# Kernel tuning notes

Hardware: AMD Instinct MI355X
Metric: run time of the kernel (lower is better)

## Reference

```python
import jax, jax.numpy as jnp
import numpy as np

D_MODEL = 1024
B, T = 4, 2048
NEG = -1000000000.0


def setup_inputs() -> dict:
    key = jax.random.key(0)
    kq, kk, kv = jax.random.split(key, 3)
    query = jax.random.normal(kq, (B, T, D_MODEL), dtype=jnp.float32)
    k = jax.random.normal(kk, (B, T, D_MODEL), dtype=jnp.float32)
    value = jax.random.normal(kv, (B, T, D_MODEL), dtype=jnp.float32)
    # causal mask: 1.0 where attention is disallowed (strictly upper triangular)
    mask = jnp.triu(jnp.ones((T, T), dtype=jnp.float32), k=1)
    return {"query": query, "key": k, "value": value, "mask": mask}


def reference(query, key, value, mask):
    # dk = sqrt(1/d_model); logits = QK^T / dk  (i.e. * sqrt(d_model)) -- faithful to source
    dk = jnp.sqrt(jnp.float32(1.0) / jnp.float32(D_MODEL))
    attn_logits = jnp.einsum("btc,bsc->bts", query, key) / dk
    attn_logits = attn_logits + mask * NEG  # mask broadcasts over batch
    score = jax.nn.softmax(attn_logits, axis=-1)
    attention = jnp.einsum("bts,bsc->btc", score, value)
    return attention
```

## Files before the change

kernel.cpp:

```cpp
#include <hip/hip_runtime.h>

#define BB 4
#define TT 2048
#define DD 1024
#define SCALE 32.0f
#define NTILE 136
#define L2E 1.4426950408889634f

typedef _Float16 f16;
typedef __attribute__((ext_vector_type(4))) _Float16 half4v;
typedef __attribute__((ext_vector_type(8))) _Float16 half8v;
typedef __attribute__((ext_vector_type(16))) float f32x16;

typedef const __attribute__((address_space(1))) unsigned int* gas_u32;
typedef __attribute__((address_space(3))) unsigned int* las_u32;

static __device__ inline void gload16(const void* g, void* l) {
    __builtin_amdgcn_global_load_lds((gas_u32)g, (las_u32)l, 16, 0, 0);
}

static __device__ inline half8v ld_frag(const f16* p) {
    half4v a = *(const half4v*)p;
    half4v b = *(const half4v*)(p + 4);
    half8v r;
    r[0] = a[0]; r[1] = a[1]; r[2] = a[2]; r[3] = a[3];
    r[4] = b[0]; r[5] = b[1]; r[6] = b[2]; r[7] = b[3];
    return r;
}


__global__ __launch_bounds__(256) void repack_qk(const float* __restrict__ Q,
                                                 const float* __restrict__ K,
                                                 f16* __restrict__ Qt,
                                                 f16* __restrict__ Kt) {
    __shared__ char rl[32768];
    int bid = blockIdx.x;
    int which = bid >> 10, b = (bid >> 8) & 3, mi = (bid >> 4) & 15, ks4 = bid & 15;
    const float* src = which ? K : Q;
    f16* dst = which ? Kt : Qt;
    float sc = which ? 1.0f : SCALE;

    int tid = threadIdx.x;
    int r = tid >> 1, h = tid & 1;
    const float* p = src + ((size_t)(b * TT + mi * 128 + r)) * DD + ks4 * 64 + h * 32;
#pragma unroll
    for (int j = 0; j < 4; ++j) {
        float4 x0 = *(const float4*)(p + j * 8);
        float4 x1 = *(const float4*)(p + j * 8 + 4);
        float vv[8] = {x0.x, x0.y, x0.z, x0.w, x1.x, x1.y, x1.z, x1.w};
        half8v hi, lo;
#pragma unroll
        for (int e = 0; e < 8; ++e) {
            float x = vv[e] * sc;
            f16 hh = (f16)x;
            hi[e] = hh;
            lo[e] = (f16)(x - (float)hh);
        }
        int ckl = h * 2 + (j >> 1);
        int shalf = j & 1;
        *(half8v*)(rl + ckl * 8192 + shalf * 2048 + r * 16) = hi;
        *(half8v*)(rl + ckl * 8192 + (2 + shalf) * 2048 + r * 16) = lo;
    }
    __syncthreads();
    char* gout = (char*)dst + ((size_t)((b * 16 + mi) * 64 + ks4 * 4)) * 8192 + tid * 128;
#pragma unroll
    for (int q = 0; q < 8; ++q)
        *(float4*)(gout + q * 16) = *(float4*)(rl + tid * 128 + q * 16);
}

__global__ __launch_bounds__(256) void transpose_v(const float* __restrict__ V,
                                                   f16* __restrict__ Vt) {
    __shared__ float Vs[64][129];
    int bid = blockIdx.x;
    int b = bid >> 8, kb = (bid >> 3) & 31, nj = bid & 7;
    const float* src = V + ((size_t)(b * TT + kb * 64)) * DD + nj * 128;
    int tid = threadIdx.x;
#pragma unroll
    for (int it = 0; it < 8; ++it) {
        int f4 = it * 256 + tid;
        int row = f4 >> 5, c4 = f4 & 31;
        float4 x = *(const float4*)(src + (size_t)row * DD + c4 * 4);
        Vs[row][c4 * 4 + 0] = x.x;
        Vs[row][c4 * 4 + 1] = x.y;
        Vs[row][c4 * 4 + 2] = x.z;
        Vs[row][c4 * 4 + 3] = x.w;
    }
    __syncthreads();
#pragma unroll
    for (int qq = 0; qq < 4; ++qq) {
        int q = tid * 4 + qq;
        int ckl = q >> 9, s = (q >> 7) & 3, n = q & 127;
        half8v hv;
#pragma unroll
        for (int e = 0; e < 8; ++e) hv[e] = (f16)Vs[ckl * 32 + s * 8 + e][n];
        char* out = (char*)Vt + ((size_t)((b * 8 + nj) * 64 + kb * 2 + ckl)) * 8192
                    + s * 2048 + n * 16;
        *(half8v*)out = hv;
    }
}

__global__ __launch_bounds__(256, 3) void k1_qk3(const f16* __restrict__ Qt,
                                                 const f16* __restrict__ Kt,
                                                 float* __restrict__ S) {
    __shared__ char lds[32768];

    int bid0 = blockIdx.x;
    int bid = (bid0 & 7) * (BB * NTILE / 8) + (bid0 >> 3);
    int b = bid / NTILE, rr0 = bid % NTILE;
    int mi = 0;
    while ((mi + 1) * (mi + 2) / 2 <= rr0) ++mi;
    int nj = rr0 - mi * (mi + 1) / 2;

    const char* Abase = (const char*)Qt + ((size_t)((b * 16 + mi) * 64)) * 8192;
    const char* Bbase = (const char*)Kt + ((size_t)((b * 16 + nj) * 64)) * 8192;
    float* Sb = S + (size_t)b * TT * TT + (size_t)(mi * 128) * TT + nj * 128;

    int tid = threadIdx.x;
    int lane = tid & 63;
    int wv = tid >> 6;
    int l31 = lane & 31, lhi = lane >> 5;
    int wrow = wv >> 1, wcol = wv & 1;

    int aoff[2], boff[2];
#pragma unroll
    for (int f = 0; f < 2; ++f) {
        int ra = wrow * 64 + f * 32 + l31;
        int rb = wcol * 64 + f * 32 + l31;
        aoff[f] = lhi * 2048 + ra * 16;
        boff[f] = lhi * 2048 + rb * 16;
    }
    int lane_go = wv * 2048 + lane * 16;
    int lane_lo = wv * 2048;

    f32x16 acc[2][2] = {};

#define K1_STAGE(CK, BUF)                                                       \
    {                                                                           \
        const char* ga = Abase + (size_t)(CK) * 8192 + lane_go;                 \
        const char* gb = Bbase + (size_t)(CK) * 8192 + lane_go;                 \
        char* la = lds + (BUF) * 16384 + lane_lo;                               \
        char* lb = la + 8192;                                                   \
        gload16(ga, la);                                                        \
        gload16(ga + 1024, la + 1024);                                          \
        gload16(gb, lb);                                                        \
        gload16(gb + 1024, lb + 1024);                                          \
    }

    K1_STAGE(0, 0);
    int cur = 0;
    for (int ck = 0; ck < 64; ++ck) {
        __syncthreads();
        if (ck + 1 < 64) K1_STAGE(ck + 1, cur ^ 1);
        const char* As = lds + cur * 16384;
        const char* Bs = As + 8192;
        half8v ah[2], al[2], bh[2], bl[2];
#pragma unroll
        for (int f = 0; f < 2; ++f) {
            ah[f] = *(const half8v*)(As + aoff[f]);
            al[f] = *(const half8v*)(As + aoff[f] + 4096);
            bh[f] = *(const half8v*)(Bs + boff[f]);
            bl[f] = *(const half8v*)(Bs + boff[f] + 4096);
        }
#pragma unroll
        for (int fm = 0; fm < 2; ++fm)
#pragma unroll
            for (int fn = 0; fn < 2; ++fn) {
                acc[fm][fn] = __builtin_amdgcn_mfma_f32_32x32x16_f16(ah[fm], bh[fn], acc[fm][fn], 0, 0, 0);
                acc[fm][fn] = __builtin_amdgcn_mfma_f32_32x32x16_f16(ah[fm], bl[fn], acc[fm][fn], 0, 0, 0);
                acc[fm][fn] = __builtin_amdgcn_mfma_f32_32x32x16_f16(al[fm], bh[fn], acc[fm][fn], 0, 0, 0);
            }
        cur ^= 1;
    }
#undef K1_STAGE
#pragma unroll
    for (int fm = 0; fm < 2; ++fm)
#pragma unroll
        for (int fn = 0; fn < 2; ++fn)
#pragma unroll
            for (int g = 0; g < 16; ++g) {
                int rr = (g & 3) + 8 * (g >> 2) + 4 * lhi;
                int row = wrow * 64 + fm * 32 + rr;
                int col = wcol * 64 + fn * 32 + l31;
                Sb[(size_t)row * TT + col] = acc[fm][fn][g];
            }
}

__global__ __launch_bounds__(256) void k1b3(const float* __restrict__ S,
                                            f16* __restrict__ Pt) {
    __shared__ float red[4];
    int rowid = blockIdx.x;
    int b = rowid >> 11, t = rowid & (TT - 1);
    const float* Sr = S + ((size_t)b * TT + t) * TT;
    int tid = threadIdx.x;
    int nv = t + 1;
    int mi = t >> 7, r = t & 127;
    int rowend = (mi + 1) << 7;
    int c = tid * 8;
    bool act = c < rowend;

    float v[8] = {0, 0, 0, 0, 0, 0, 0, 0};
    if (act) {
        float4 x0 = *(const float4*)(Sr + c);
        float4 x1 = *(const float4*)(Sr + c + 4);
        v[0] = x0.x; v[1] = x0.y; v[2] = x0.z; v[3] = x0.w;
        v[4] = x1.x; v[5] = x1.y; v[6] = x1.z; v[7] = x1.w;
    }

    float m = -3.0e38f;
    if (act) {
#pragma unroll
        for (int j = 0; j < 8; ++j)
            if (c + j < nv) m = fmaxf(m, v[j]);
    }
#pragma unroll
    for (int o = 32; o > 0; o >>= 1) m = fmaxf(m, __shfl_xor(m, o));
    if ((tid & 63) == 0) red[tid >> 6] = m;
    __syncthreads();
    m = fmaxf(fmaxf(red[0], red[1]), fmaxf(red[2], red[3]));
    __syncthreads();

    float e[8];
    float s = 0.f;
#pragma unroll
    for (int j = 0; j < 8; ++j) {
        e[j] = (act && c + j < nv) ? exp2f((v[j] - m) * L2E) : 0.0f;
        s += e[j];
    }
#pragma unroll
    for (int o = 32; o > 0; o >>= 1) s += __shfl_xor(s, o);
    if ((tid & 63) == 0) red[tid >> 6] = s;
    __syncthreads();
    s = red[0] + red[1] + red[2] + red[3];
    float inv = 1.0f / s;

    if (act) {
        half8v hv;
#pragma unroll
        for (int j = 0; j < 8; ++j) hv[j] = (f16)(e[j] * inv);
        int ck = c >> 5, sl = (c >> 3) & 3;
        char* dst = (char*)Pt + ((size_t)((b * 16 + mi) * 64 + ck)) * 8192
                    + sl * 2048 + r * 16;
        *(half8v*)dst = hv;
    }
}

__global__ __launch_bounds__(256, 2) void k2_pv3(const f16* __restrict__ Pt,
                                                 const f16* __restrict__ Vt,
                                                 float* __restrict__ O) {
    __shared__ char lds[49152];

    int bid0 = blockIdx.x;
    int bid = (bid0 & 7) * 32 + (bid0 >> 3);
    int b = bid >> 6, mi = (bid >> 2) & 15, nj2 = bid & 3;
    int kc = (mi + 1) * 4;

    const char* Abase = (const char*)Pt + ((size_t)((b * 16 + mi) * 64)) * 8192;
    const char* B0base = (const char*)Vt + ((size_t)((b * 8 + nj2 * 2) * 64)) * 8192;
    const char* B1base = (const char*)Vt + ((size_t)((b * 8 + nj2 * 2 + 1) * 64)) * 8192;
    float* Ob = O + (size_t)b * TT * DD + (size_t)(mi * 128) * DD + nj2 * 256;

    int tid = threadIdx.x;
    int lane = tid & 63;
    int wv = tid >> 6;
    int l31 = lane & 31, lhi = lane >> 5;
    int wr = wv >> 1, wc = wv & 1;

    f32x16 acc[2][4] = {};
    int lane16 = lane * 16;

#define K2_STAGE(CK, BUF)                                                       \
    {                                                                           \
        size_t gck = (size_t)(CK) * 8192;                                       \
        char* lb = lds + (BUF) * 24576;                                         \
        _Pragma("unroll") for (int i = 0; i < 6; ++i) {                         \
            int off = (i * 4 + wv) * 1024;                                      \
            const char* gsrc = (off < 8192) ? (Abase + gck + off)               \
                             : (off < 16384) ? (B0base + gck + off - 8192)      \
                                             : (B1base + gck + off - 16384);    \
            gload16(gsrc + lane16, lb + off);                                   \
        }                                                                       \
    }

    K2_STAGE(0, 0);
    int cur = 0;
    for (int ck = 0; ck < kc; ++ck) {
        __syncthreads();
        if (ck + 1 < kc) K2_STAGE(ck + 1, cur ^ 1);
        const char* As = lds + cur * 24576;
        const char* Bs = As + 8192 + wc * 8192;
#pragma unroll
        for (int ks = 0; ks < 2; ++ks) {
            int slot = (ks * 2 + lhi) * 2048;
            half8v a0 = *(const half8v*)(As + slot + (wr * 64 + l31) * 16);
            half8v a1 = *(const half8v*)(As + slot + (wr * 64 + 32 + l31) * 16);
            half8v b0 = *(const half8v*)(Bs + slot + (l31) * 16);
            half8v b1 = *(const half8v*)(Bs + slot + (32 + l31) * 16);
            half8v b2 = *(const half8v*)(Bs + slot + (64 + l31) * 16);
            half8v b3 = *(const half8v*)(Bs + slot + (96 + l31) * 16);
            acc[0][0] = __builtin_amdgcn_mfma_f32_32x32x16_f16(a0, b0, acc[0][0], 0, 0, 0);
            acc[0][1] = __builtin_amdgcn_mfma_f32_32x32x16_f16(a0, b1, acc[0][1], 0, 0, 0);
            acc[0][2] = __builtin_amdgcn_mfma_f32_32x32x16_f16(a0, b2, acc[0][2], 0, 0, 0);
            acc[0][3] = __builtin_amdgcn_mfma_f32_32x32x16_f16(a0, b3, acc[0][3], 0, 0, 0);
            acc[1][0] = __builtin_amdgcn_mfma_f32_32x32x16_f16(a1, b0, acc[1][0], 0, 0, 0);
            acc[1][1] = __builtin_amdgcn_mfma_f32_32x32x16_f16(a1, b1, acc[1][1], 0, 0, 0);
            acc[1][2] = __builtin_amdgcn_mfma_f32_32x32x16_f16(a1, b2, acc[1][2], 0, 0, 0);
            acc[1][3] = __builtin_amdgcn_mfma_f32_32x32x16_f16(a1, b3, acc[1][3], 0, 0, 0);
        }
        cur ^= 1;
    }
#undef K2_STAGE
#pragma unroll
    for (int fm = 0; fm < 2; ++fm)
#pragma unroll
        for (int fn = 0; fn < 4; ++fn)
#pragma unroll
            for (int g = 0; g < 16; ++g) {
                int rr = (g & 3) + 8 * (g >> 2) + 4 * lhi;
                int row = wr * 64 + fm * 32 + rr;
                int col = wc * 128 + fn * 32 + l31;
                Ob[(size_t)row * DD + col] = acc[fm][fn][g];
            }
}

__global__ __launch_bounds__(256, 2) void k1_qk(const float* __restrict__ Q,
                                                const float* __restrict__ Kmat,
                                                float* __restrict__ S) {
    __shared__ f16 Ah[128][36], Al[128][36], Bh[128][36], Bl[128][36];
    int bid = blockIdx.x;
    int b = bid / NTILE, r = bid % NTILE;
    int mi = 0;
    while ((mi + 1) * (mi + 2) / 2 <= r) ++mi;
    int nj = r - mi * (mi + 1) / 2;
    const float* Qb = Q + ((size_t)b * TT + (size_t)mi * 128) * DD;
    const float* Kb = Kmat + ((size_t)b * TT + (size_t)nj * 128) * DD;
    float* Sb = S + (size_t)b * TT * TT + (size_t)(mi * 128) * TT + nj * 128;
    int tid = threadIdx.x;
    int lane = tid & 63;
    int wave = tid >> 6;
    int l31 = lane & 31, lhi = lane >> 5;
    int wrow = wave >> 1, wcol = wave & 1;
    int r0 = tid >> 1;
    int c0 = (tid & 1) * 16;
    f32x16 acc[2][2] = {};
    float4 abuf[4], bbuf[4];
#pragma unroll
    for (int j = 0; j < 4; ++j) {
        abuf[j] = *(const float4*)(Qb + (size_t)r0 * DD + c0 + 4 * j);
        bbuf[j] = *(const float4*)(Kb + (size_t)r0 * DD + c0 + 4 * j);
    }
    for (int ch = 0; ch < DD / 32; ++ch) {
        __syncthreads();
#pragma unroll
        for (int j = 0; j < 4; ++j) {
            float4 a = abuf[j], bq = bbuf[j];
            float ax[4] = {a.x * SCALE, a.y * SCALE, a.z * SCALE, a.w * SCALE};
            float bx[4] = {bq.x, bq.y, bq.z, bq.w};
            half4v ahv, alv, bhv, blv;
#pragma unroll
            for (int e = 0; e < 4; ++e) {
                f16 h = (f16)ax[e];
                ahv[e] = h;
                alv[e] = (f16)(ax[e] - (float)h);
                f16 g = (f16)bx[e];
                bhv[e] = g;
                blv[e] = (f16)(bx[e] - (float)g);
            }
            *(half4v*)&Ah[r0][c0 + 4 * j] = ahv;
            *(half4v*)&Al[r0][c0 + 4 * j] = alv;
            *(half4v*)&Bh[r0][c0 + 4 * j] = bhv;
            *(half4v*)&Bl[r0][c0 + 4 * j] = blv;
        }
        __syncthreads();
        if (ch + 1 < DD / 32) {
            int ck = (ch + 1) * 32;
#pragma unroll
            for (int j = 0; j < 4; ++j) {
                abuf[j] = *(const float4*)(Qb + (size_t)r0 * DD + ck + c0 + 4 * j);
                bbuf[j] = *(const float4*)(Kb + (size_t)r0 * DD + ck + c0 + 4 * j);
            }
        }
#pragma unroll
        for (int ks = 0; ks < 2; ++ks) {
            int kb = ks * 16 + lhi * 8;
            half8v ahf[2], alf[2], bhf[2], blf[2];
#pragma unroll
            for (int f = 0; f < 2; ++f) {
                ahf[f] = ld_frag(&Ah[wrow * 64 + f * 32 + l31][kb]);
                alf[f] = ld_frag(&Al[wrow * 64 + f * 32 + l31][kb]);
                bhf[f] = ld_frag(&Bh[wcol * 64 + f * 32 + l31][kb]);
                blf[f] = ld_frag(&Bl[wcol * 64 + f * 32 + l31][kb]);
            }
#pragma unroll
            for (int fm = 0; fm < 2; ++fm)
#pragma unroll
                for (int fn = 0; fn < 2; ++fn) {
                    acc[fm][fn] = __builtin_amdgcn_mfma_f32_32x32x16_f16(ahf[fm], bhf[fn], acc[fm][fn], 0, 0, 0);
                    acc[fm][fn] = __builtin_amdgcn_mfma_f32_32x32x16_f16(ahf[fm], blf[fn], acc[fm][fn], 0, 0, 0);
                    acc[fm][fn] = __builtin_amdgcn_mfma_f32_32x32x16_f16(alf[fm], bhf[fn], acc[fm][fn], 0, 0, 0);
                }
        }
    }
#pragma unroll
    for (int fm = 0; fm < 2; ++fm)
#pragma unroll
        for (int fn = 0; fn < 2; ++fn)
#pragma unroll
            for (int g = 0; g < 16; ++g) {
                int rr = (g & 3) + 8 * (g >> 2) + 4 * lhi;
                int row = wrow * 64 + fm * 32 + rr;
                int col = wcol * 64 + fn * 32 + l31;
                Sb[(size_t)row * TT + col] = acc[fm][fn][g];
            }
}

__global__ __launch_bounds__(256) void k1b_softmax(const float* __restrict__ S,
                                                   f16* __restrict__ P) {
    __shared__ float red[4];
    int rowid = blockIdx.x;
    int b = rowid >> 11, t = rowid & (TT - 1);
    const float* Sr = S + (size_t)b * TT * TT + (size_t)t * TT;
    f16* Pr = P + (size_t)b * TT * TT + (size_t)t * TT;
    int tid = threadIdx.x;
    int nv = t + 1;
    int rowend = ((t >> 7) + 1) << 7;
    float m = -3.0e38f;
    for (int c = tid; c < nv; c += 256) m = fmaxf(m, Sr[c]);
#pragma unroll
    for (int o = 32; o > 0; o >>= 1) m = fmaxf(m, __shfl_xor(m, o));
    if ((tid & 63) == 0) red[tid >> 6] = m;
    __syncthreads();
    m = fmaxf(fmaxf(red[0], red[1]), fmaxf(red[2], red[3]));
    __syncthreads();
    float s = 0.f;
    for (int c = tid; c < nv; c += 256) s += exp2f((Sr[c] - m) * L2E);
#pragma unroll
    for (int o = 32; o > 0; o >>= 1) s += __shfl_xor(s, o);
    if ((tid & 63) == 0) red[tid >> 6] = s;
    __syncthreads();
    s = red[0] + red[1] + red[2] + red[3];
    float inv = 1.0f / s;
    for (int c = tid; c < rowend; c += 256) {
        float p = (c < nv) ? exp2f((Sr[c] - m) * L2E) * inv : 0.0f;
        Pr[c] = (f16)p;
    }
}

__global__ __launch_bounds__(256, 2) void k2_pv(const f16* __restrict__ P,
                                                const float* __restrict__ V,
                                                float* __restrict__ O) {
    __shared__ f16 Pa[128][36];
    __shared__ f16 Vtt[128][36];
    int bid = blockIdx.x;
    int b = bid >> 7;
    int rest = bid & 127;
    int mi = rest >> 3, nj = rest & 7;
    int kend = (mi + 1) * 128;
    const f16* Pb = P + (size_t)b * TT * TT + (size_t)(mi * 128) * TT;
    const float* Vb = V + (size_t)b * TT * DD + nj * 128;
    float* Ob = O + (size_t)b * TT * DD + (size_t)(mi * 128) * DD + nj * 128;
    int tid = threadIdx.x;
    int lane = tid & 63;
    int wave = tid >> 6;
    int l31 = lane & 31, lhi = lane >> 5;
    int wrow = wave >> 1, wcol = wave & 1;
    f32x16 acc[2][2] = {};
    int pr = tid >> 1, pc = (tid & 1) * 16;
    int vk = tid >> 3, vn = (tid & 7) * 16;
    uint2 pbuf[4];
    float4 vbuf[4];
#pragma unroll
    for (int j = 0; j < 4; ++j) {
        pbuf[j] = *(const uint2*)(Pb + (size_t)pr * TT + pc + 4 * j);
        vbuf[j] = *(const float4*)(Vb + (size_t)vk * DD + vn + 4 * j);
    }
    for (int ck = 0; ck < kend; ck += 32) {
        __syncthreads();
#pragma unroll
        for (int j = 0; j < 4; ++j) {
            *(uint2*)&Pa[pr][pc + 4 * j] = pbuf[j];
            float4 v = vbuf[j];
            float vv[4] = {v.x, v.y, v.z, v.w};
            int n0 = vn + 4 * j;
#pragma unroll
            for (int e = 0; e < 4; ++e) {
                int n = n0 + e;
                Vtt[n][vk ^ ((((unsigned)n >> 4) & 3) << 3)] = (f16)vv[e];
            }
        }
        __syncthreads();
        if (ck + 32 < kend) {
            int cn = ck + 32;
#pragma unroll
            for (int j = 0; j < 4; ++j) {
                pbuf[j] = *(const uint2*)(Pb + (size_t)pr * TT + cn + pc + 4 * j);
                vbuf[j] = *(const float4*)(Vb + (size_t)(cn + vk) * DD + vn + 4 * j);
            }
        }
#pragma unroll
        for (int ks = 0; ks < 2; ++ks) {
            int kb = ks * 16 + lhi * 8;
            half8v paf[2], vbf[2];
#pragma unroll
            for (int f = 0; f < 2; ++f) {
                paf[f] = ld_frag(&Pa[wrow * 64 + f * 32 + l31][kb]);
                int n = wcol * 64 + f * 32 + l31;
                int kbs = kb ^ ((((unsigned)n >> 4) & 3) << 3);
                vbf[f] = ld_frag(&Vtt[n][kbs]);
            }
#pragma unroll
            for (int fm = 0; fm < 2; ++fm)
#pragma unroll
                for (int fn = 0; fn < 2; ++fn)
                    acc[fm][fn] = __builtin_amdgcn_mfma_f32_32x32x16_f16(paf[fm], vbf[fn], acc[fm][fn], 0, 0, 0);
        }
    }
#pragma unroll
    for (int fm = 0; fm < 2; ++fm)
#pragma unroll
        for (int fn = 0; fn < 2; ++fn)
#pragma unroll
            for (int g = 0; g < 16; ++g) {
                int rr = (g & 3) + 8 * (g >> 2) + 4 * lhi;
                int row = wrow * 64 + fm * 32 + rr;
                int col = wcol * 64 + fn * 32 + l31;
                Ob[(size_t)row * DD + col] = acc[fm][fn][g];
            }
}

__global__ __launch_bounds__(256) void fa_fallback(const float* __restrict__ Q,
                                                   const float* __restrict__ Kmat,
                                                   const float* __restrict__ V,
                                                   float* __restrict__ O) {
    __shared__ float qs[DD];
    __shared__ float osum[DD];
    __shared__ float red[4];
    int rowid = blockIdx.x;
    int b = rowid >> 11, t = rowid & (TT - 1);
    const float* q = Q + ((size_t)b * TT + t) * DD;
    int tid = threadIdx.x;
    for (int j = tid; j < DD; j += 256) { qs[j] = q[j] * SCALE; osum[j] = 0.f; }
    __syncthreads();
    float m = -3.0e38f, l = 0.f;
    for (int s = 0; s <= t; ++s) {
        const float* kr = Kmat + ((size_t)b * TT + s) * DD;
        float part = 0.f;
#pragma unroll
        for (int j = 0; j < 4; ++j) part += qs[tid * 4 + j] * kr[tid * 4 + j];
#pragma unroll
        for (int o = 32; o > 0; o >>= 1) part += __shfl_xor(part, o);
        if ((tid & 63) == 0) red[tid >> 6] = part;
        __syncthreads();
        float dot = red[0] + red[1] + red[2] + red[3];
        float mn = fmaxf(m, dot);
        float f = exp2f((m - mn) * 1.44269504f);
        float e = exp2f((dot - mn) * 1.44269504f);
        l = l * f + e;
        const float* vr = V + ((size_t)b * TT + s) * DD;
#pragma unroll
        for (int j = 0; j < 4; ++j) {
            int c = tid * 4 + j;
            osum[c] = osum[c] * f + e * vr[c];
        }
        m = mn;
        __syncthreads();
    }
    float inv = 1.f / l;
    for (int j = tid; j < DD; j += 256) O[((size_t)b * TT + t) * DD + j] = osum[j] * inv;
}

extern "C" void kernel_launch(void* const* d_in, const int* in_sizes, int n_in,
                              void* d_out, int out_size, void* d_ws, size_t ws_size,
                              hipStream_t stream) {
    const float* Q = (const float*)d_in[0];
    const float* K = (const float*)d_in[1];
    const float* V = (const float*)d_in[2];
    float* O = (float*)d_out;

    const size_t MB = 1024 * 1024;
    const size_t QT_B = 32 * MB, KT_B = 32 * MB, VT_B = 16 * MB, S_B = 64 * MB;
    const size_t FULL = QT_B + KT_B + VT_B + S_B;

    size_t sbytes = (size_t)BB * TT * TT * 4;
    size_t pbytes = (size_t)BB * TT * TT * 2;

    if (ws_size >= FULL) {
        f16* Qt = (f16*)d_ws;
        f16* Kt = (f16*)((char*)d_ws + QT_B);
        f16* Vt = (f16*)((char*)d_ws + QT_B + KT_B);
        float* S = (float*)((char*)d_ws + QT_B + KT_B + VT_B);
        f16* Pt = (f16*)d_ws;
        hipLaunchKernelGGL(repack_qk, dim3(2048), dim3(256), 0, stream, Q, K, Qt, Kt);
        hipLaunchKernelGGL(transpose_v, dim3(1024), dim3(256), 0, stream, V, Vt);
        hipLaunchKernelGGL(k1_qk3, dim3(BB * NTILE), dim3(256), 0, stream, Qt, Kt, S);
        hipLaunchKernelGGL(k1b3, dim3(BB * TT), dim3(256), 0, stream, S, Pt);
        hipLaunchKernelGGL(k2_pv3, dim3(256), dim3(256), 0, stream, Pt, Vt, O);
    } else if (ws_size >= sbytes + pbytes) {
        float* S = (float*)d_ws;
        f16* P = (f16*)((char*)d_ws + sbytes);
        hipLaunchKernelGGL(k1_qk, dim3(BB * NTILE), dim3(256), 0, stream, Q, K, S);
        hipLaunchKernelGGL(k1b_softmax, dim3(BB * TT), dim3(256), 0, stream, S, P);
        hipLaunchKernelGGL(k2_pv, dim3(BB * 16 * 8), dim3(256), 0, stream, P, V, O);
    } else {
        hipLaunchKernelGGL(fa_fallback, dim3(BB * TT), dim3(256), 0, stream, Q, K, V, O);
    }
}
```

Before: 171.6 us.

## Split K reduction across two wave groups in QK and PV GEMMs

Both GEMM kernels now launch 512 threads per block, and the two halves of the waves each handle half of the reduction dimension. Their partial accumulators are combined through LDS before the store. PV also moves to 128x128 output tiles with twice as many blocks, which gives more waves per CU for the few, uneven causal tiles. The cost is extra LDS traffic and a barrier for the final reduction, plus 64KB of LDS per block, which may limit how many blocks fit on a CU.

Result: no change. 170.8 us (-0.5%).

```diff
diff --git a/kernel.cpp b/kernel.cpp
--- a/kernel.cpp
+++ b/kernel.cpp
@@ -99,10 +99,10 @@
     }
 }
 
-__global__ __launch_bounds__(256, 3) void k1_qk3(const f16* __restrict__ Qt,
+__global__ __launch_bounds__(512, 4) void k1_qk4(const f16* __restrict__ Qt,
                                                  const f16* __restrict__ Kt,
                                                  float* __restrict__ S) {
-    __shared__ char lds[32768];
+    __shared__ char lds[65536];
 
     int bid0 = blockIdx.x;
     int bid = (bid0 & 7) * (BB * NTILE / 8) + (bid0 >> 3);
@@ -118,27 +118,30 @@
     int tid = threadIdx.x;
     int lane = tid & 63;
     int wv = tid >> 6;
+    int kh = wv >> 2;
+    int wq = wv & 3;
     int l31 = lane & 31, lhi = lane >> 5;
-    int wrow = wv >> 1, wcol = wv & 1;
+    int wrow = wq >> 1, wcol = wq & 1;
 
     int aoff[2], boff[2];
 #pragma unroll
     for (int f = 0; f < 2; ++f) {
-        int ra = wrow * 64 + f * 32 + l31;
-        int rb = wcol * 64 + f * 32 + l31;
-        aoff[f] = lhi * 2048 + ra * 16;
-        boff[f] = lhi * 2048 + rb * 16;
-    }
-    int lane_go = wv * 2048 + lane * 16;
-    int lane_lo = wv * 2048;
+        aoff[f] = lhi * 2048 + (wrow * 64 + f * 32 + l31) * 16;
+        boff[f] = lhi * 2048 + (wcol * 64 + f * 32 + l31) * 16;
+    }
+    int lane_go = wq * 2048 + lane * 16;
+    int lane_lo = wq * 2048;
+    char* lds_h = lds + kh * 32768;
+    const char* Ab = Abase + (size_t)kh * 32 * 8192;
+    const char* Bb = Bbase + (size_t)kh * 32 * 8192;
 
     f32x16 acc[2][2] = {};
 
-#define K1_STAGE(CK, BUF)                                                       \
+#define K1_STAGE(IT, BUF)                                                       \
     {                                                                           \
-        const char* ga = Abase + (size_t)(CK) * 8192 + lane_go;                 \
-        const char* gb = Bbase + (size_t)(CK) * 8192 + lane_go;                 \
-        char* la = lds + (BUF) * 16384 + lane_lo;                               \
+        const char* ga = Ab + (size_t)(IT) * 8192 + lane_go;                    \
+        const char* gb = Bb + (size_t)(IT) * 8192 + lane_go;                    \
+        char* la = lds_h + (BUF) * 16384 + lane_lo;                             \
         char* lb = la + 8192;                                                   \
         gload16(ga, la);                                                        \
         gload16(ga + 1024, la + 1024);                                          \
@@ -148,10 +151,10 @@
 
     K1_STAGE(0, 0);
     int cur = 0;
-    for (int ck = 0; ck < 64; ++ck) {
-        __syncthreads();
-        if (ck + 1 < 64) K1_STAGE(ck + 1, cur ^ 1);
-        const char* As = lds + cur * 16384;
+    for (int it = 0; it < 32; ++it) {
+        __syncthreads();
+        if (it + 1 < 32) K1_STAGE(it + 1, cur ^ 1);
+        const char* As = lds_h + cur * 16384;
         const char* Bs = As + 8192;
         half8v ah[2], al[2], bh[2], bl[2];
 #pragma unroll
@@ -172,17 +175,34 @@
         cur ^= 1;
     }
 #undef K1_STAGE
-#pragma unroll
-    for (int fm = 0; fm < 2; ++fm)
-#pragma unroll
-        for (int fn = 0; fn < 2; ++fn)
-#pragma unroll
-            for (int g = 0; g < 16; ++g) {
-                int rr = (g & 3) + 8 * (g >> 2) + 4 * lhi;
-                int row = wrow * 64 + fm * 32 + rr;
-                int col = wcol * 64 + fn * 32 + l31;
-                Sb[(size_t)row * TT + col] = acc[fm][fn][g];
-            }
+
+    __syncthreads();
+    if (kh) {
+#pragma unroll
+        for (int fm = 0; fm < 2; ++fm)
+#pragma unroll
+            for (int fn = 0; fn < 2; ++fn)
+#pragma unroll
+                for (int g = 0; g < 16; ++g)
+                    *(float*)(lds + wq * 16384 + (fm * 2 + fn) * 4096 + g * 256 + lane * 4)
+                        = acc[fm][fn][g];
+    }
+    __syncthreads();
+    if (!kh) {
+#pragma unroll
+        for (int fm = 0; fm < 2; ++fm)
+#pragma unroll
+            for (int fn = 0; fn < 2; ++fn)
+#pragma unroll
+                for (int g = 0; g < 16; ++g) {
+                    float v = acc[fm][fn][g]
+                        + *(const float*)(lds + wq * 16384 + (fm * 2 + fn) * 4096 + g * 256 + lane * 4);
+                    int rr = (g & 3) + 8 * (g >> 2) + 4 * lhi;
+                    int row = wrow * 64 + fm * 32 + rr;
+                    int col = wcol * 64 + fn * 32 + l31;
+                    Sb[(size_t)row * TT + col] = v;
+                }
+    }
 }
 
 __global__ __launch_bounds__(256) void k1b3(const float* __restrict__ S,
@@ -244,82 +264,104 @@
     }
 }
 
-__global__ __launch_bounds__(256, 2) void k2_pv3(const f16* __restrict__ Pt,
+__global__ __launch_bounds__(512, 4) void k2_pv4(const f16* __restrict__ Pt,
                                                  const f16* __restrict__ Vt,
                                                  float* __restrict__ O) {
-    __shared__ char lds[49152];
+    __shared__ char lds[65536];
 
     int bid0 = blockIdx.x;
-    int bid = (bid0 & 7) * 32 + (bid0 >> 3);
-    int b = bid >> 6, mi = (bid >> 2) & 15, nj2 = bid & 3;
-    int kc = (mi + 1) * 4;
+    int bid = (bid0 & 7) * 64 + (bid0 >> 3);
+    int b = bid >> 7, mi = (bid >> 3) & 15, nj = bid & 7;
+    int kch = (mi + 1) * 2;
 
     const char* Abase = (const char*)Pt + ((size_t)((b * 16 + mi) * 64)) * 8192;
-    const char* B0base = (const char*)Vt + ((size_t)((b * 8 + nj2 * 2) * 64)) * 8192;
-    const char* B1base = (const char*)Vt + ((size_t)((b * 8 + nj2 * 2 + 1) * 64)) * 8192;
-    float* Ob = O + (size_t)b * TT * DD + (size_t)(mi * 128) * DD + nj2 * 256;
+    const char* Bbase = (const char*)Vt + ((size_t)((b * 8 + nj) * 64)) * 8192;
+    float* Ob = O + (size_t)b * TT * DD + (size_t)(mi * 128) * DD + nj * 128;
 
     int tid = threadIdx.x;
     int lane = tid & 63;
     int wv = tid >> 6;
+    int kh = wv >> 2;
+    int wq = wv & 3;
     int l31 = lane & 31, lhi = lane >> 5;
-    int wr = wv >> 1, wc = wv & 1;
-
-    f32x16 acc[2][4] = {};
-    int lane16 = lane * 16;
-
-#define K2_STAGE(CK, BUF)                                                       \
+    int wrow = wq >> 1, wcol = wq & 1;
+
+    int arow[2], brow[2];
+#pragma unroll
+    for (int f = 0; f < 2; ++f) {
+        arow[f] = (wrow * 64 + f * 32 + l31) * 16;
+        brow[f] = (wcol * 64 + f * 32 + l31) * 16;
+    }
+    int lane_go = wq * 2048 + lane * 16;
+    int lane_lo = wq * 2048;
+    char* lds_h = lds + kh * 32768;
+    const char* Ab = Abase + (size_t)kh * kch * 8192;
+    const char* Bb = Bbase + (size_t)kh * kch * 8192;
+
+    f32x16 acc[2][2] = {};
+
+#define K2_STAGE(IT, BUF)                                                       \
     {                                                                           \
-        size_t gck = (size_t)(CK) * 8192;                                       \
-        char* lb = lds + (BUF) * 24576;                                         \
-        _Pragma("unroll") for (int i = 0; i < 6; ++i) {                         \
-            int off = (i * 4 + wv) * 1024;                                      \
-            const char* gsrc = (off < 8192) ? (Abase + gck + off)               \
-                             : (off < 16384) ? (B0base + gck + off - 8192)      \
-                                             : (B1base + gck + off - 16384);    \
-            gload16(gsrc + lane16, lb + off);                                   \
-        }                                                                       \
+        const char* ga = Ab + (size_t)(IT) * 8192 + lane_go;                    \
+        const char* gb = Bb + (size_t)(IT) * 8192 + lane_go;                    \
+        char* la = lds_h + (BUF) * 16384 + lane_lo;                             \
+        char* lb = la + 8192;                                                   \
+        gload16(ga, la);                                                        \
+        gload16(ga + 1024, la + 1024);                                          \
+        gload16(gb, lb);                                                        \
+        gload16(gb + 1024, lb + 1024);                                          \
     }
 
     K2_STAGE(0, 0);
     int cur = 0;
-    for (int ck = 0; ck < kc; ++ck) {
-        __syncthreads();
-        if (ck + 1 < kc) K2_STAGE(ck + 1, cur ^ 1);
-        const char* As = lds + cur * 24576;
-        const char* Bs = As + 8192 + wc * 8192;
+    for (int it = 0; it < kch; ++it) {
+        __syncthreads();
+        if (it + 1 < kch) K2_STAGE(it + 1, cur ^ 1);
+        const char* As = lds_h + cur * 16384;
+        const char* Bs = As + 8192;
 #pragma unroll
         for (int ks = 0; ks < 2; ++ks) {
             int slot = (ks * 2 + lhi) * 2048;
-            half8v a0 = *(const half8v*)(As + slot + (wr * 64 + l31) * 16);
-            half8v a1 = *(const half8v*)(As + slot + (wr * 64 + 32 + l31) * 16);
-            half8v b0 = *(const half8v*)(Bs + slot + (l31) * 16);
-            half8v b1 = *(const half8v*)(Bs + slot + (32 + l31) * 16);
-            half8v b2 = *(const half8v*)(Bs + slot + (64 + l31) * 16);
-            half8v b3 = *(const half8v*)(Bs + slot + (96 + l31) * 16);
+            half8v a0 = *(const half8v*)(As + slot + arow[0]);
+            half8v a1 = *(const half8v*)(As + slot + arow[1]);
+            half8v b0 = *(const half8v*)(Bs + slot + brow[0]);
+            half8v b1 = *(const half8v*)(Bs + slot + brow[1]);
             acc[0][0] = __builtin_amdgcn_mfma_f32_32x32x16_f16(a0, b0, acc[0][0], 0, 0, 0);
             acc[0][1] = __builtin_amdgcn_mfma_f32_32x32x16_f16(a0, b1, acc[0][1], 0, 0, 0);
-            acc[0][2] = __builtin_amdgcn_mfma_f32_32x32x16_f16(a0, b2, acc[0][2], 0, 0, 0);
-            acc[0][3] = __builtin_amdgcn_mfma_f32_32x32x16_f16(a0, b3, acc[0][3], 0, 0, 0);
             acc[1][0] = __builtin_amdgcn_mfma_f32_32x32x16_f16(a1, b0, acc[1][0], 0, 0, 0);
             acc[1][1] = __builtin_amdgcn_mfma_f32_32x32x16_f16(a1, b1, acc[1][1], 0, 0, 0);
-            acc[1][2] = __builtin_amdgcn_mfma_f32_32x32x16_f16(a1, b2, acc[1][2], 0, 0, 0);
-            acc[1][3] = __builtin_amdgcn_mfma_f32_32x32x16_f16(a1, b3, acc[1][3], 0, 0, 0);
         }
         cur ^= 1;
     }
 #undef K2_STAGE
-#pragma unroll
-    for (int fm = 0; fm < 2; ++fm)
-#pragma unroll
-        for (int fn = 0; fn < 4; ++fn)
-#pragma unroll
-            for (int g = 0; g < 16; ++g) {
-                int rr = (g & 3) + 8 * (g >> 2) + 4 * lhi;
-                int row = wr * 64 + fm * 32 + rr;
-                int col = wc * 128 + fn * 32 + l31;
-                Ob[(size_t)row * DD + col] = acc[fm][fn][g];
-            }
+
+    __syncthreads();
+    if (kh) {
+#pragma unroll
+        for (int fm = 0; fm < 2; ++fm)
+#pragma unroll
+            for (int fn = 0; fn < 2; ++fn)
+#pragma unroll
+                for (int g = 0; g < 16; ++g)
+                    *(float*)(lds + wq * 16384 + (fm * 2 + fn) * 4096 + g * 256 + lane * 4)
+                        = acc[fm][fn][g];
+    }
+    __syncthreads();
+    if (!kh) {
+#pragma unroll
+        for (int fm = 0; fm < 2; ++fm)
+#pragma unroll
+            for (int fn = 0; fn < 2; ++fn)
+#pragma unroll
+                for (int g = 0; g < 16; ++g) {
+                    float v = acc[fm][fn][g]
+                        + *(const float*)(lds + wq * 16384 + (fm * 2 + fn) * 4096 + g * 256 + lane * 4);
+                    int rr = (g & 3) + 8 * (g >> 2) + 4 * lhi;
+                    int row = wrow * 64 + fm * 32 + rr;
+                    int col = wcol * 64 + fn * 32 + l31;
+                    Ob[(size_t)row * DD + col] = v;
+                }
+    }
 }
 
 __global__ __launch_bounds__(256, 2) void k1_qk(const float* __restrict__ Q,
@@ -591,9 +633,9 @@
         f16* Pt = (f16*)d_ws;
         hipLaunchKernelGGL(repack_qk, dim3(2048), dim3(256), 0, stream, Q, K, Qt, Kt);
         hipLaunchKernelGGL(transpose_v, dim3(1024), dim3(256), 0, stream, V, Vt);
-        hipLaunchKernelGGL(k1_qk3, dim3(BB * NTILE), dim3(256), 0, stream, Qt, Kt, S);
+        hipLaunchKernelGGL(k1_qk4, dim3(BB * NTILE), dim3(512), 0, stream, Qt, Kt, S);
         hipLaunchKernelGGL(k1b3, dim3(BB * TT), dim3(256), 0, stream, S, Pt);
-        hipLaunchKernelGGL(k2_pv3, dim3(256), dim3(256), 0, stream, Pt, Vt, O);
+        hipLaunchKernelGGL(k2_pv4, dim3(512), dim3(512), 0, stream, Pt, Vt, O);
     } else if (ws_size >= sbytes + pbytes) {
         float* S = (float*)d_ws;
         f16* P = (f16*)((char*)d_ws + sbytes);
```

## Triple-buffer QK and PV GEMM loads and halve PV tile width

Applied to the files above, without the earlier changes.

Both GEMM kernels move from a double-buffered LDS pipeline with __syncthreads to a three-stage ring. Loads are issued two chunks ahead, and the code waits with explicit vmcnt counts plus a raw s_barrier, so more global-to-LDS latency can be hidden. The PV kernel's output tile shrinks from 128x256 to 128x128, doubling the grid to 512 blocks, with occupancy raised to 3 blocks per CU. The smaller tile improves load balance on the causal triangle but re-reads P twice as often. The QK kernel's LDS grows to 48KB, which may limit its 3-block occupancy.

Result: faster. 164.1 us (-4.4%).

```diff
diff --git a/kernel.cpp b/kernel.cpp
--- a/kernel.cpp
+++ b/kernel.cpp
@@ -99,10 +99,10 @@
     }
 }
 
-__global__ __launch_bounds__(256, 3) void k1_qk3(const f16* __restrict__ Qt,
+__global__ __launch_bounds__(256, 3) void k1_qk5(const f16* __restrict__ Qt,
                                                  const f16* __restrict__ Kt,
                                                  float* __restrict__ S) {
-    __shared__ char lds[32768];
+    __shared__ char lds[49152];
 
     int bid0 = blockIdx.x;
     int bid = (bid0 & 7) * (BB * NTILE / 8) + (bid0 >> 3);
@@ -124,10 +124,8 @@
     int aoff[2], boff[2];
 #pragma unroll
     for (int f = 0; f < 2; ++f) {
-        int ra = wrow * 64 + f * 32 + l31;
-        int rb = wcol * 64 + f * 32 + l31;
-        aoff[f] = lhi * 2048 + ra * 16;
-        boff[f] = lhi * 2048 + rb * 16;
+        aoff[f] = lhi * 2048 + (wrow * 64 + f * 32 + l31) * 16;
+        boff[f] = lhi * 2048 + (wcol * 64 + f * 32 + l31) * 16;
     }
     int lane_go = wv * 2048 + lane * 16;
     int lane_lo = wv * 2048;
@@ -147,11 +145,15 @@
     }
 
     K1_STAGE(0, 0);
-    int cur = 0;
+    K1_STAGE(1, 1);
+    int cb = 0;
+    int sb = 2;
     for (int ck = 0; ck < 64; ++ck) {
-        __syncthreads();
-        if (ck + 1 < 64) K1_STAGE(ck + 1, cur ^ 1);
-        const char* As = lds + cur * 16384;
+        if (ck < 63) asm volatile("s_waitcnt vmcnt(4)" ::: "memory");
+        else         asm volatile("s_waitcnt vmcnt(0)" ::: "memory");
+        __builtin_amdgcn_s_barrier();
+        if (ck + 2 < 64) K1_STAGE(ck + 2, sb);
+        const char* As = lds + cb * 16384;
         const char* Bs = As + 8192;
         half8v ah[2], al[2], bh[2], bl[2];
 #pragma unroll
@@ -169,7 +171,8 @@
                 acc[fm][fn] = __builtin_amdgcn_mfma_f32_32x32x16_f16(ah[fm], bl[fn], acc[fm][fn], 0, 0, 0);
                 acc[fm][fn] = __builtin_amdgcn_mfma_f32_32x32x16_f16(al[fm], bh[fn], acc[fm][fn], 0, 0, 0);
             }
-        cur ^= 1;
+        cb = (cb == 2) ? 0 : cb + 1;
+        sb = (sb == 2) ? 0 : sb + 1;
     }
 #undef K1_STAGE
 #pragma unroll
@@ -244,80 +247,84 @@
     }
 }
 
-__global__ __launch_bounds__(256, 2) void k2_pv3(const f16* __restrict__ Pt,
+__global__ __launch_bounds__(256, 3) void k2_pv5(const f16* __restrict__ Pt,
                                                  const f16* __restrict__ Vt,
                                                  float* __restrict__ O) {
     __shared__ char lds[49152];
 
     int bid0 = blockIdx.x;
-    int bid = (bid0 & 7) * 32 + (bid0 >> 3);
-    int b = bid >> 6, mi = (bid >> 2) & 15, nj2 = bid & 3;
-    int kc = (mi + 1) * 4;
+    int bid = (bid0 & 7) * 64 + (bid0 >> 3);
+    int b = bid >> 7, mi = (bid >> 3) & 15, nj = bid & 7;
+    int kch = (mi + 1) * 4;
 
     const char* Abase = (const char*)Pt + ((size_t)((b * 16 + mi) * 64)) * 8192;
-    const char* B0base = (const char*)Vt + ((size_t)((b * 8 + nj2 * 2) * 64)) * 8192;
-    const char* B1base = (const char*)Vt + ((size_t)((b * 8 + nj2 * 2 + 1) * 64)) * 8192;
-    float* Ob = O + (size_t)b * TT * DD + (size_t)(mi * 128) * DD + nj2 * 256;
+    const char* Bbase = (const char*)Vt + ((size_t)((b * 8 + nj) * 64)) * 8192;
+    float* Ob = O + (size_t)b * TT * DD + (size_t)(mi * 128) * DD + nj * 128;
 
     int tid = threadIdx.x;
     int lane = tid & 63;
     int wv = tid >> 6;
     int l31 = lane & 31, lhi = lane >> 5;
-    int wr = wv >> 1, wc = wv & 1;
-
-    f32x16 acc[2][4] = {};
-    int lane16 = lane * 16;
+    int wrow = wv >> 1, wcol = wv & 1;
+
+    int arow[2], brow[2];
+#pragma unroll
+    for (int f = 0; f < 2; ++f) {
+        arow[f] = (wrow * 64 + f * 32 + l31) * 16;
+        brow[f] = (wcol * 64 + f * 32 + l31) * 16;
+    }
+    int lane_go = wv * 2048 + lane * 16;
+    int lane_lo = wv * 2048;
+
+    f32x16 acc[2][2] = {};
 
 #define K2_STAGE(CK, BUF)                                                       \
     {                                                                           \
-        size_t gck = (size_t)(CK) * 8192;                                       \
-        char* lb = lds + (BUF) * 24576;                                         \
-        _Pragma("unroll") for (int i = 0; i < 6; ++i) {                         \
-            int off = (i * 4 + wv) * 1024;                                      \
-            const char* gsrc = (off < 8192) ? (Abase + gck + off)               \
-                             : (off < 16384) ? (B0base + gck + off - 8192)      \
-                                             : (B1base + gck + off - 16384);    \
-            gload16(gsrc + lane16, lb + off);                                   \
-        }                                                                       \
+        const char* ga = Abase + (size_t)(CK) * 8192 + lane_go;                 \
+        const char* gb = Bbase + (size_t)(CK) * 8192 + lane_go;                 \
+        char* la = lds + (BUF) * 16384 + lane_lo;                               \
+        char* lb = la + 8192;                                                   \
+        gload16(ga, la);                                                        \
+        gload16(ga + 1024, la + 1024);                                          \
+        gload16(gb, lb);                                                        \
+        gload16(gb + 1024, lb + 1024);                                          \
     }
 
     K2_STAGE(0, 0);
-    int cur = 0;
-    for (int ck = 0; ck < kc; ++ck) {
-        __syncthreads();
-        if (ck + 1 < kc) K2_STAGE(ck + 1, cur ^ 1);
-        const char* As = lds + cur * 24576;
-        const char* Bs = As + 8192 + wc * 8192;
+    K2_STAGE(1, 1);
+    int cb = 0, sb = 2;
+    for (int it = 0; it < kch; ++it) {
+        if (it + 1 < kch) asm volatile("s_waitcnt vmcnt(4)" ::: "memory");
+        else              asm volatile("s_waitcnt vmcnt(0)" ::: "memory");
+        __builtin_amdgcn_s_barrier();
+        if (it + 2 < kch) K2_STAGE(it + 2, sb);
+        const char* As = lds + cb * 16384;
+        const char* Bs = As + 8192;
 #pragma unroll
         for (int ks = 0; ks < 2; ++ks) {
             int slot = (ks * 2 + lhi) * 2048;
-            half8v a0 = *(const half8v*)(As + slot + (wr * 64 + l31) * 16);
-            half8v a1 = *(const half8v*)(As + slot + (wr * 64 + 32 + l31) * 16);
-            half8v b0 = *(const half8v*)(Bs + slot + (l31) * 16);
-            half8v b1 = *(const half8v*)(Bs + slot + (32 + l31) * 16);
-            half8v b2 = *(const half8v*)(Bs + slot + (64 + l31) * 16);
-            half8v b3 = *(const half8v*)(Bs + slot + (96 + l31) * 16);
+            half8v a0 = *(const half8v*)(As + slot + arow[0]);
+            half8v a1 = *(const half8v*)(As + slot + arow[1]);
+            half8v b0 = *(const half8v*)(Bs + slot + brow[0]);
+            half8v b1 = *(const half8v*)(Bs + slot + brow[1]);
             acc[0][0] = __builtin_amdgcn_mfma_f32_32x32x16_f16(a0, b0, acc[0][0], 0, 0, 0);
             acc[0][1] = __builtin_amdgcn_mfma_f32_32x32x16_f16(a0, b1, acc[0][1], 0, 0, 0);
-            acc[0][2] = __builtin_amdgcn_mfma_f32_32x32x16_f16(a0, b2, acc[0][2], 0, 0, 0);
-            acc[0][3] = __builtin_amdgcn_mfma_f32_32x32x16_f16(a0, b3, acc[0][3], 0, 0, 0);
             acc[1][0] = __builtin_amdgcn_mfma_f32_32x32x16_f16(a1, b0, acc[1][0], 0, 0, 0);
             acc[1][1] = __builtin_amdgcn_mfma_f32_32x32x16_f16(a1, b1, acc[1][1], 0, 0, 0);
-            acc[1][2] = __builtin_amdgcn_mfma_f32_32x32x16_f16(a1, b2, acc[1][2], 0, 0, 0);
-            acc[1][3] = __builtin_amdgcn_mfma_f32_32x32x16_f16(a1, b3, acc[1][3], 0, 0, 0);
-        }
-        cur ^= 1;
+        }
+        cb = (cb == 2) ? 0 : cb + 1;
+        sb = (sb == 2) ? 0 : sb + 1;
     }
 #undef K2_STAGE
 #pragma unroll
     for (int fm = 0; fm < 2; ++fm)
 #pragma unroll
-        for (int fn = 0; fn < 4; ++fn)
+        for (int fn = 0; fn < 2; ++fn)
 #pragma unroll
             for (int g = 0; g < 16; ++g) {
                 int rr = (g & 3) + 8 * (g >> 2) + 4 * lhi;
-                int row = wr * 64 + fm * 32 + rr;
-                int col = wc * 128 + fn * 32 + l31;
+                int row = wrow * 64 + fm * 32 + rr;
+                int col = wcol * 64 + fn * 32 + l31;
                 Ob[(size_t)row * DD + col] = acc[fm][fn][g];
             }
 }
@@ -591,9 +598,9 @@
         f16* Pt = (f16*)d_ws;
         hipLaunchKernelGGL(repack_qk, dim3(2048), dim3(256), 0, stream, Q, K, Qt, Kt);
         hipLaunchKernelGGL(transpose_v, dim3(1024), dim3(256), 0, stream, V, Vt);
-        hipLaunchKernelGGL(k1_qk3, dim3(BB * NTILE), dim3(256), 0, stream, Qt, Kt, S);
+        hipLaunchKernelGGL(k1_qk5, dim3(BB * NTILE), dim3(256), 0, stream, Qt, Kt, S);
         hipLaunchKernelGGL(k1b3, dim3(BB * TT), dim3(256), 0, stream, S, Pt);
-        hipLaunchKernelGGL(k2_pv3, dim3(256), dim3(256), 0, stream, Pt, Vt, O);
+        hipLaunchKernelGGL(k2_pv5, dim3(512), dim3(256), 0, stream, Pt, Vt, O);
     } else if (ws_size >= sbytes + pbytes) {
         float* S = (float*)d_ws;
         f16* P = (f16*)((char*)d_ws + sbytes);
```
